# Optimization experiments

Hardware: AMD Instinct MI355X
Metric: run time of the kernel (lower is better)

Reference implementation:

```python
import jax, jax.numpy as jnp
import numpy as np

H = 16          # n_heads
DH = 128        # head_dim
DR = 64         # rope_dim
DC = DH - DR    # content_dim = 64
THETA = 10000.0
SCALE = 1.0 / np.sqrt(DH)


def _rope_tables(T, dtype):
    inv = 1.0 / (THETA ** (jnp.arange(0, DR, 2, dtype=jnp.float32) / DR))  # [DR/2]
    t = jnp.arange(T, dtype=jnp.float32)
    freqs = jnp.outer(t, inv)  # [T, DR/2]
    return jnp.cos(freqs).astype(dtype), jnp.sin(freqs).astype(dtype)


def _apply_rope(x, cos, sin):
    # x: [B,H,T,DR]; cos/sin: [T,DR/2] broadcast over B,H
    d = x.shape[-1] // 2
    x1, x2 = x[..., :d], x[..., d:]
    return jnp.concatenate([x1 * cos - x2 * sin, x1 * sin + x2 * cos], axis=-1)


def setup_inputs() -> dict:
    key = jax.random.key(0)
    ks = jax.random.split(key, 9)
    B, T, D = 1, 2048, 2048
    s = 0.02
    return {
        "x": jax.random.normal(ks[0], (B, T, D), jnp.float32),
        "Wq_down": jax.random.normal(ks[1], (D, 512), jnp.float32) * s,
        "Wq_up": jax.random.normal(ks[2], (512, H * DC), jnp.float32) * s,
        "Wq_rope": jax.random.normal(ks[3], (D, H * DR), jnp.float32) * s,
        "Wkv_down": jax.random.normal(ks[4], (D, 512), jnp.float32) * s,
        "Wk_up": jax.random.normal(ks[5], (512, H * DC), jnp.float32) * s,
        "Wv_up": jax.random.normal(ks[6], (512, H * DH), jnp.float32) * s,
        "Wk_rope": jax.random.normal(ks[7], (D, H * DR), jnp.float32) * s,
        "Wo": jax.random.normal(ks[8], (H * DH, D), jnp.float32) * s,
    }


def reference(x, Wq_down, Wq_up, Wq_rope, Wkv_down, Wk_up, Wv_up, Wk_rope, Wo):
    B, T, D = x.shape
    # low-rank query path: down then up, content part only
    q_content = ((x @ Wq_down) @ Wq_up).reshape(B, T, H, DC).transpose(0, 2, 1, 3)
    q_pos = (x @ Wq_rope).reshape(B, T, H, DR).transpose(0, 2, 1, 3)
    kv_latent = x @ Wkv_down                    # [B,T,d_latent]
    k_pos = (x @ Wk_rope).reshape(B, T, H, DR).transpose(0, 2, 1, 3)

    cos, sin = _rope_tables(T, x.dtype)
    q_pos = _apply_rope(q_pos, cos, sin)
    k_pos = _apply_rope(k_pos, cos, sin)

    k_content = (kv_latent @ Wk_up).reshape(B, T, H, DC).transpose(0, 2, 1, 3)
    v = (kv_latent @ Wv_up).reshape(B, T, H, DH).transpose(0, 2, 1, 3)

    q = jnp.concatenate([q_content, q_pos], axis=-1)  # [B,H,T,DH]
    k = jnp.concatenate([k_content, k_pos], axis=-1)  # [B,H,T,DH]

    scores = jnp.einsum("bhtd,bhsd->bhts", q, k) * SCALE
    causal = jnp.tril(jnp.ones((T, T), dtype=bool))
    scores = jnp.where(causal, scores, jnp.finfo(scores.dtype).min)
    attn = jax.nn.softmax(scores, axis=-1)
    out = jnp.einsum("bhts,bhsd->bhtd", attn, v)       # [B,H,T,DH]
    out = out.transpose(0, 2, 1, 3).reshape(B, T, H * DH)
    return out @ Wo
```

## Files before the change

kernel.cpp:

```cpp
#include <hip/hip_runtime.h>
#include <math.h>

#define T_SEQ 2048
#define D_MODEL 2048
#define H_HEADS 16
#define DH 128
#define DR 64
#define DC 64
#define D_LAT 512
#define NSPLIT 3
#define QSCALE (0.08838834764831845f * 1.4426950408889634f)

typedef __attribute__((ext_vector_type(8))) short short8;
typedef __attribute__((ext_vector_type(4))) short short4v;
typedef __attribute__((ext_vector_type(4))) float f32x4;

#if __has_builtin(__builtin_amdgcn_exp2f)
#define EXP2(x) __builtin_amdgcn_exp2f(x)
#else
#define EXP2(x) exp2f(x)
#endif

__device__ __forceinline__ float bf2f(short b) {
    unsigned u = ((unsigned)(unsigned short)b) << 16;
    return __builtin_bit_cast(float, u);
}
__device__ __forceinline__ short f2bf(float f) {
    unsigned u = __builtin_bit_cast(unsigned, f);
    unsigned r = u + 0x7fffu + ((u >> 16) & 1u);
    return (short)(r >> 16);
}
__device__ __forceinline__ short f2bf_trunc(float f) {
    return (short)(__builtin_bit_cast(unsigned, f) >> 16);
}

#define GLD_LDS(gp, lp) \
    __builtin_amdgcn_global_load_lds( \
        (const __attribute__((address_space(1))) void*)(gp), \
        (__attribute__((address_space(3))) void*)(lp), 16, 0, 0)

__device__ __forceinline__ void ct_tile(float (*tile)[33],
                                        const float* __restrict__ W,
                                        short* __restrict__ Wt,
                                        int R, int C, int ldo, int rel) {
    int bx = rel % (C / 32), by = rel / (C / 32);
    int c0 = bx * 32, r0 = by * 32;
    int tx = threadIdx.x & 31, ty = threadIdx.x >> 5;
    #pragma unroll
    for (int i = 0; i < 4; ++i)
        tile[ty + i * 8][tx] = W[(size_t)(r0 + ty + i * 8) * C + c0 + tx];
    __syncthreads();
    #pragma unroll
    for (int i = 0; i < 4; ++i)
        Wt[(size_t)(c0 + ty + i * 8) * ldo + r0 + tx] = f2bf(tile[tx][ty + i * 8]);
    __syncthreads();
}

__global__ __launch_bounds__(256) void prep(const float* __restrict__ x,
                                            short* __restrict__ xb,
                                            const float* __restrict__ Wqd,
                                            const float* __restrict__ Wkvd,
                                            const float* __restrict__ Wqr,
                                            const float* __restrict__ Wkr,
                                            const float* __restrict__ Wqu,
                                            const float* __restrict__ Wku,
                                            const float* __restrict__ Wvu,
                                            const float* __restrict__ Wo,
                                            short* __restrict__ WdT,
                                            short* __restrict__ WupT2,
                                            short* __restrict__ WoT) {
    __shared__ float tile[32][33];
    int bid = blockIdx.x;
    if (bid < 4096) {
        int i = bid * 1024 + threadIdx.x * 4;
        float4 f = *(const float4*)&x[i];
        short4v o;
        o.x = f2bf(f.x); o.y = f2bf(f.y); o.z = f2bf(f.z); o.w = f2bf(f.w);
        *(short4v*)&xb[i] = o;
    } else if (bid < 5120) {
        ct_tile(tile, Wqd,  WdT + (size_t)0 * 2048,    2048, 512,  2048, bid - 4096);
    } else if (bid < 6144) {
        ct_tile(tile, Wkvd, WdT + (size_t)512 * 2048,  2048, 512,  2048, bid - 5120);
    } else if (bid < 8192) {
        ct_tile(tile, Wqr,  WdT + (size_t)1024 * 2048, 2048, 1024, 2048, bid - 6144);
    } else if (bid < 10240) {
        ct_tile(tile, Wkr,  WdT + (size_t)2048 * 2048, 2048, 1024, 2048, bid - 8192);
    } else if (bid < 10752) {
        ct_tile(tile, Wqu,  WupT2 + (size_t)0 * 512,    512, 1024, 512, bid - 10240);
    } else if (bid < 11264) {
        ct_tile(tile, Wku,  WupT2 + (size_t)1024 * 512, 512, 1024, 512, bid - 10752);
    } else if (bid < 12288) {
        ct_tile(tile, Wvu,  WupT2 + (size_t)2048 * 512, 512, 2048, 512, bid - 11264);
    } else {
        ct_tile(tile, Wo,   WoT, 2048, 2048, 2048, bid - 12288);
    }
}

__global__ __launch_bounds__(256) void transpose_bf16(const short* __restrict__ in,
                                                      short* __restrict__ outb,
                                                      int ldi) {
    __shared__ short tile[64][65];
    int c0 = blockIdx.x * 64, t0 = blockIdx.y * 64;
    int tx = threadIdx.x & 31, ty = threadIdx.x >> 5;
    #pragma unroll
    for (int i = 0; i < 8; ++i) {
        int r = ty + i * 8;
        int vv = *(const int*)&in[(size_t)(t0 + r) * ldi + c0 + tx * 2];
        tile[r][tx * 2]     = (short)(vv & 0xffff);
        tile[r][tx * 2 + 1] = (short)(((unsigned)vv) >> 16);
    }
    __syncthreads();
    #pragma unroll
    for (int i = 0; i < 8; ++i) {
        int c = ty + i * 8;
        unsigned lo = (unsigned short)tile[tx * 2][c];
        unsigned hi = (unsigned short)tile[tx * 2 + 1][c];
        *(int*)&outb[(size_t)(c0 + c) * 2048 + t0 + tx * 2] = (int)(lo | (hi << 16));
    }
}

__global__ __launch_bounds__(256) void gemm_bt(const short* __restrict__ A,
                                               const short* __restrict__ A2,
                                               const short* __restrict__ Bt,
                                               short* __restrict__ C0,
                                               short* __restrict__ C1,
                                               short* __restrict__ C2,
                                               short* __restrict__ C3,
                                               int N, int Kblk,
                                               int lda, int ldb, int ldc,
                                               int ncut, int scut, float cscale) {
    __shared__ short As[128 * 32];
    __shared__ short Bs[128 * 32];
    const int tid = threadIdx.x;
    const int wave = tid >> 6, lane = tid & 63;
    const int lin = blockIdx.x;
    const int X = N >> 7, Xq = X >> 2;
    const int xcd = lin & 7;
    int r = lin >> 3;
    const int bx = (xcd & 3) * Xq + (r % Xq); r /= Xq;
    const int by = (xcd >> 2) * 8 + (r & 7);
    const int bz = r >> 3;
    const int row0 = by * 128, col0 = bx * 128;
    const int kbase = bz * Kblk;
    const short* Ause = (col0 < ncut) ? A : A2;
    short* Cuse = (bz == 0) ? C0 : (bz == 1) ? C1 : (bz == 2) ? C2 : C3;
    const int wr = (wave >> 1) * 64, wc = (wave & 1) * 64;
    const int lr = lane & 15, quad = lane >> 4;

    f32x4 acc[4][4];
    #pragma unroll
    for (int i = 0; i < 4; ++i)
        #pragma unroll
        for (int j = 0; j < 4; ++j) acc[i][j] = (f32x4){0.f, 0.f, 0.f, 0.f};

    for (int k0 = kbase; k0 < kbase + Kblk; k0 += 32) {
        __syncthreads();
        #pragma unroll
        for (int it = 0; it < 2; ++it) {
            int idx = wave * 64 + it * 256 + lane;
            const short* ga = Ause + (size_t)(row0 + (idx >> 2)) * lda + k0 + (idx & 3) * 8;
            const short* gb = Bt   + (size_t)(col0 + (idx >> 2)) * ldb + k0 + (idx & 3) * 8;
            int lds0 = (wave * 64 + it * 256) * 8;
            GLD_LDS(ga, &As[lds0]);
            GLD_LDS(gb, &Bs[lds0]);
        }
        __syncthreads();

        short8 af[4], bfr[4];
        #pragma unroll
        for (int i = 0; i < 4; ++i)
            af[i] = *(const short8*)&As[(wr + i * 16 + lr) * 32 + quad * 8];
        #pragma unroll
        for (int j = 0; j < 4; ++j)
            bfr[j] = *(const short8*)&Bs[(wc + j * 16 + lr) * 32 + quad * 8];
        #pragma unroll
        for (int i = 0; i < 4; ++i)
            #pragma unroll
            for (int j = 0; j < 4; ++j)
                acc[i][j] = __builtin_amdgcn_mfma_f32_16x16x32_bf16(af[i], bfr[j],
                                                                   acc[i][j], 0, 0, 0);
    }

    const float sc = (col0 < scut) ? cscale : 1.0f;
    #pragma unroll
    for (int i = 0; i < 4; ++i) {
        int rb = row0 + wr + i * 16 + quad * 4;
        #pragma unroll
        for (int j = 0; j < 4; ++j) {
            int c = col0 + wc + j * 16 + lr;
            #pragma unroll
            for (int rr = 0; rr < 4; ++rr)
                Cuse[(size_t)(rb + rr) * ldc + c] = f2bf(acc[i][j][rr] * sc);
        }
    }
}

__global__ __launch_bounds__(192) void finish_down(short* __restrict__ cat,
                                                   const short* __restrict__ pdown) {
    const int t = blockIdx.x;
    const int k8 = threadIdx.x * 8;
    const int c0 = ((k8 >> 5) << 6) + (k8 & 31);
    const size_t lo = (size_t)t * 3072 + c0;
    const size_t hi = lo + 32;
    short8 al = *(const short8*)&cat[lo];
    short8 ah = *(const short8*)&cat[hi];
    short8 bl = *(const short8*)&pdown[lo];
    short8 bh = *(const short8*)&pdown[hi];
    float xl[8], xh[8];
    #pragma unroll
    for (int j = 0; j < 8; ++j) {
        xl[j] = bf2f(al[j]) + bf2f(bl[j]);
        xh[j] = bf2f(ah[j]) + bf2f(bh[j]);
    }
    if (c0 >= 1024) {
        float sc = (c0 < 2048) ? QSCALE : 1.0f;
        #pragma unroll
        for (int j = 0; j < 8; ++j) {
            int i = (c0 & 31) + j;
            float freq = (float)t * __powf(10000.0f, -(float)i / 32.0f);
            float cs = cosf(freq), sn = sinf(freq);
            float r1 = (xl[j] * cs - xh[j] * sn) * sc;
            float r2 = (xl[j] * sn + xh[j] * cs) * sc;
            xl[j] = r1; xh[j] = r2;
        }
    }
    short8 ol, oh;
    #pragma unroll
    for (int j = 0; j < 8; ++j) { ol[j] = f2bf(xl[j]); oh[j] = f2bf(xh[j]); }
    *(short8*)&cat[lo] = ol;
    *(short8*)&cat[hi] = oh;
}

__global__ __launch_bounds__(256) void add_out_f32(const short* __restrict__ p0,
                                                   const short* __restrict__ p1,
                                                   const short* __restrict__ p2,
                                                   const short* __restrict__ p3,
                                                   float* __restrict__ out) {
    int i = (blockIdx.x * 256 + threadIdx.x) * 4;
    short4v a = *(const short4v*)&p0[i];
    short4v b = *(const short4v*)&p1[i];
    short4v c = *(const short4v*)&p2[i];
    short4v d = *(const short4v*)&p3[i];
    float4 o;
    o.x = (bf2f(a.x) + bf2f(b.x)) + (bf2f(c.x) + bf2f(d.x));
    o.y = (bf2f(a.y) + bf2f(b.y)) + (bf2f(c.y) + bf2f(d.y));
    o.z = (bf2f(a.z) + bf2f(b.z)) + (bf2f(c.z) + bf2f(d.z));
    o.w = (bf2f(a.w) + bf2f(b.w)) + (bf2f(c.w) + bf2f(d.w));
    *(float4*)&out[i] = o;
}

__global__ __launch_bounds__(256) void attn_mla_split(const short* __restrict__ qkup,
                                                      const short* __restrict__ cat,
                                                      const short* __restrict__ vT,
                                                      short* __restrict__ Opart01,
                                                      short* __restrict__ Opart2,
                                                      float* __restrict__ lpart) {
    const int lin = blockIdx.x;
    const int xcd = lin & 7;
    int r_ = lin >> 3;
    const int h = xcd + 8 * (r_ & 1);
    r_ >>= 1;
    const int qt = 31 - (r_ & 31);
    const int g = r_ >> 5;
    const int tid = threadIdx.x;
    const int wave = tid >> 6, lane = tid & 63;
    const int lr = lane & 15, quad = lane >> 4;

    __shared__ short Ks[32 * 128];
    __shared__ short Vst[128 * 32];
    __shared__ short Ps[4][16 * 40];

    short* Og = (g < 2) ? Opart01 + (size_t)g * (T_SEQ * 2048) : Opart2;
    const short8 ones = {0x3F80, 0x3F80, 0x3F80, 0x3F80,
                         0x3F80, 0x3F80, 0x3F80, 0x3F80};

    const int Q0 = qt * 64;
    const int qrow0 = Q0 + wave * 16;
    const int nchunk = 2 * qt + 2;
    const int qmax = qrow0 + 15;

    short8 qf[4];
    {
        int t = qrow0 + lr;
        #pragma unroll
        for (int kci = 0; kci < 4; ++kci) {
            const short* src = (kci < 2)
                ? qkup + (size_t)t * 4096 + h * 64
                : cat + (size_t)t * 3072 + 1024 + h * 64;
            qf[kci] = *(const short8*)&src[(kci & 1) * 32 + quad * 8];
        }
    }

    const int idx = wave * 64 + lane;
    const int key = idx >> 4;
    const int cg = (idx & 15) ^ (key & 15);
    const short* kp0 = (cg < 8)
        ? qkup + (size_t)key * 4096 + 1024 + h * 64 + cg * 8
        : cat + (size_t)key * 3072 + 2048 + h * 64 + (cg - 8) * 8;
    const int kst = (cg < 8) ? 4096 : 3072;
    const short* kp1 = kp0 + (size_t)16 * kst;
    const int dd = idx >> 2;
    const int scg = (idx & 3) ^ (dd & 3);
    const short* vp0 = vT + (size_t)(h * 128 + dd) * 2048 + scg * 8;
    const short* vp1 = vp0 + (size_t)64 * 2048;
    kp0 += (size_t)g * 32 * kst; kp1 += (size_t)g * 32 * kst;
    vp0 += g * 32;               vp1 += g * 32;
    const int kadv = NSPLIT * 32 * kst;
    const int vadv = NSPLIT * 32;
    const int ldsA = (wave * 64) * 8;
    const int ldsB = (wave * 64 + 256) * 8;

    f32x4 Oacc[8];
    #pragma unroll
    for (int d = 0; d < 8; ++d) Oacc[d] = (f32x4){0.f, 0.f, 0.f, 0.f};
    f32x4 Lacc = (f32x4){0.f, 0.f, 0.f, 0.f};

    for (int c = g; c < nchunk; c += NSPLIT) {
        const int s0 = c * 32;
        __syncthreads();
        GLD_LDS(kp0, &Ks[ldsA]);
        GLD_LDS(kp1, &Ks[ldsB]);
        GLD_LDS(vp0, &Vst[ldsA]);
        GLD_LDS(vp1, &Vst[ldsB]);
        kp0 += kadv; kp1 += kadv; vp0 += vadv; vp1 += vadv;
        __syncthreads();
        if (s0 > qmax) continue;

        f32x4 sacc[2];
        #pragma unroll
        for (int n = 0; n < 2; ++n) {
            sacc[n] = (f32x4){0.f, 0.f, 0.f, 0.f};
            #pragma unroll
            for (int kci = 0; kci < 4; ++kci) {
                short8 kf = *(const short8*)
                    &Ks[(n * 16 + lr) * 128 + ((kci * 4 + quad) ^ lr) * 8];
                sacc[n] = __builtin_amdgcn_mfma_f32_16x16x32_bf16(qf[kci], kf,
                                                                 sacc[n], 0, 0, 0);
            }
        }
        if (s0 + 31 > qrow0) {
            #pragma unroll
            for (int r = 0; r < 4; ++r) {
                int qg = qrow0 + quad * 4 + r;
                #pragma unroll
                for (int n = 0; n < 2; ++n) {
                    int s = s0 + n * 16 + lr;
                    sacc[n][r] = (s <= qg) ? sacc[n][r] : -1e30f;
                }
            }
        }
        #pragma unroll
        for (int r = 0; r < 4; ++r) {
            Ps[wave][(quad * 4 + r) * 40 + lr]      = f2bf_trunc(EXP2(sacc[0][r]));
            Ps[wave][(quad * 4 + r) * 40 + 16 + lr] = f2bf_trunc(EXP2(sacc[1][r]));
        }
        short8 pf = *(const short8*)&Ps[wave][lr * 40 + quad * 8];
        Lacc = __builtin_amdgcn_mfma_f32_16x16x32_bf16(pf, ones, Lacc, 0, 0, 0);
        #pragma unroll
        for (int dt = 0; dt < 8; ++dt) {
            short8 vf = *(const short8*)
                &Vst[(dt * 16 + lr) * 32 + (quad ^ (lr & 3)) * 8];
            Oacc[dt] = __builtin_amdgcn_mfma_f32_16x16x32_bf16(pf, vf,
                                                              Oacc[dt], 0, 0, 0);
        }
    }

    #pragma unroll
    for (int r = 0; r < 4; ++r) {
        int t = qrow0 + quad * 4 + r;
        #pragma unroll
        for (int dt = 0; dt < 8; ++dt)
            Og[(size_t)t * 2048 + h * 128 + dt * 16 + lr] = f2bf(Oacc[dt][r]);
    }
    if (lr == 0) {
        #pragma unroll
        for (int r = 0; r < 4; ++r) {
            int t = qrow0 + quad * 4 + r;
            lpart[(size_t)(g * T_SEQ + t) * H_HEADS + h] = Lacc[r];
        }
    }
}

__global__ __launch_bounds__(256) void attn_combine(const short* __restrict__ O01,
                                                    const short* __restrict__ O2,
                                                    const float* __restrict__ lpart,
                                                    short* __restrict__ ao) {
    const int t = blockIdx.x;
    const int h = threadIdx.x >> 4;
    const int di = (threadIdx.x & 15) * 8;
    size_t off = (size_t)t * 2048 + h * 128 + di;
    short8 a = *(const short8*)&O01[off];
    short8 b = *(const short8*)&O01[(size_t)T_SEQ * 2048 + off];
    short8 c = *(const short8*)&O2[off];
    float den = lpart[(size_t)(0 * T_SEQ + t) * H_HEADS + h] +
                lpart[(size_t)(1 * T_SEQ + t) * H_HEADS + h] +
                lpart[(size_t)(2 * T_SEQ + t) * H_HEADS + h];
    float inv = 1.0f / den;
    short8 o;
    #pragma unroll
    for (int j = 0; j < 8; ++j)
        o[j] = f2bf((bf2f(a[j]) + bf2f(b[j]) + bf2f(c[j])) * inv);
    *(short8*)&ao[off] = o;
}

extern "C" void kernel_launch(void* const* d_in, const int* in_sizes, int n_in,
                              void* d_out, int out_size, void* d_ws, size_t ws_size,
                              hipStream_t stream) {
    const float* x        = (const float*)d_in[0];
    const float* Wq_down  = (const float*)d_in[1];
    const float* Wq_up    = (const float*)d_in[2];
    const float* Wq_rope  = (const float*)d_in[3];
    const float* Wkv_down = (const float*)d_in[4];
    const float* Wk_up    = (const float*)d_in[5];
    const float* Wv_up    = (const float*)d_in[6];
    const float* Wk_rope  = (const float*)d_in[7];
    const float* Wo       = (const float*)d_in[8];
    float* out = (float*)d_out;

    short* p = (short*)d_ws;
    short* xb     = p; p += (size_t)2048 * 2048;
    short* WoT    = p; p += (size_t)2048 * 2048;
    short* cat    = p; p += (size_t)2048 * 3072;
    short* upcat2 = p; p += (size_t)2048 * 4096;
    short* WdT    = p; p += (size_t)3072 * 2048;
    short* WupT2  = p; p += (size_t)4096 * 512;
    short* vT     = p; p += (size_t)2048 * 2048;
    float* lpart  = (float*)p;
    short* pdown   = upcat2;
    short* aob     = cat;
    short* Opart01 = WdT;
    short* Opart2  = xb;
    short* pw0     = upcat2;
    short* pw1     = upcat2 + (size_t)2048 * 2048;
    short* pw2     = WdT;
    short* pw3     = WdT + (size_t)2048 * 2048;

    prep<<<dim3(16384), 256, 0, stream>>>(x, xb, Wq_down, Wkv_down, Wq_rope,
                                          Wk_rope, Wq_up, Wk_up, Wv_up, Wo,
                                          WdT, WupT2, WoT);

    gemm_bt<<<dim3(24 * 16 * 2), 256, 0, stream>>>(xb, xb, WdT, cat, pdown,
                                                   nullptr, nullptr,
                                                   3072, 1024,
                                                   2048, 2048, 3072, 1 << 30, 0, 1.f);

    finish_down<<<dim3(2048), 192, 0, stream>>>(cat, pdown);

    gemm_bt<<<dim3(32 * 16 * 1), 256, 0, stream>>>(cat, cat + 512, WupT2,
                                                   upcat2, nullptr, nullptr, nullptr,
                                                   4096, 512,
                                                   3072, 512, 4096, 1024, 1024, QSCALE);

    transpose_bf16<<<dim3(32, 32), 256, 0, stream>>>(upcat2 + 2048, vT, 4096);

    attn_mla_split<<<dim3(32 * 16 * NSPLIT), 256, 0, stream>>>(upcat2, cat, vT,
                                                               Opart01, Opart2, lpart);
    attn_combine<<<dim3(2048), 256, 0, stream>>>(Opart01, Opart2, lpart, aob);

    gemm_bt<<<dim3(16 * 16 * 4), 256, 0, stream>>>(aob, aob, WoT, pw0, pw1, pw2, pw3,
                                                   2048, 512,
                                                   2048, 2048, 2048, 1 << 30, 0, 1.f);
    add_out_f32<<<dim3(2048 * 2048 / 1024), 256, 0, stream>>>(pw0, pw1, pw2, pw3, out);
}
```

Measured before the change: 285.9 us.

## Process 128 query rows per attention block to reuse K/V tiles

The split attention kernel now gives each wave two 16-row query sub-blocks, so each block covers 128 query rows instead of 64 and the grid is halved. Every K/V chunk loaded into LDS then feeds twice the MFMA work, which cuts global and LDS traffic per unit of compute. In exchange it uses more registers for the doubled accumulators, launches fewer blocks, and idles the lower sub-block on diagonal chunks, which adds imbalance. The RoPE step also switches to fast intrinsic sin and cos, trading some accuracy for cheaper math.

```diff
diff --git a/kernel.cpp b/kernel.cpp
--- a/kernel.cpp
+++ b/kernel.cpp
@@ -218,7 +218,7 @@
         for (int j = 0; j < 8; ++j) {
             int i = (c0 & 31) + j;
             float freq = (float)t * __powf(10000.0f, -(float)i / 32.0f);
-            float cs = cosf(freq), sn = sinf(freq);
+            float cs = __cosf(freq), sn = __sinf(freq);
             float r1 = (xl[j] * cs - xh[j] * sn) * sc;
             float r2 = (xl[j] * sn + xh[j] * cs) * sc;
             xl[j] = r1; xh[j] = r2;
@@ -260,34 +260,35 @@
     int r_ = lin >> 3;
     const int h = xcd + 8 * (r_ & 1);
     r_ >>= 1;
-    const int qt = 31 - (r_ & 31);
-    const int g = r_ >> 5;
+    const int qt2 = 15 - (r_ & 15);
+    const int g = r_ >> 4;
     const int tid = threadIdx.x;
     const int wave = tid >> 6, lane = tid & 63;
     const int lr = lane & 15, quad = lane >> 4;
 
     __shared__ short Ks[32 * 128];
     __shared__ short Vst[128 * 32];
-    __shared__ short Ps[4][16 * 40];
+    __shared__ short Ps[4][2][16 * 40];
 
     short* Og = (g < 2) ? Opart01 + (size_t)g * (T_SEQ * 2048) : Opart2;
     const short8 ones = {0x3F80, 0x3F80, 0x3F80, 0x3F80,
                          0x3F80, 0x3F80, 0x3F80, 0x3F80};
 
-    const int Q0 = qt * 64;
-    const int qrow0 = Q0 + wave * 16;
-    const int nchunk = 2 * qt + 2;
-    const int qmax = qrow0 + 15;
-
-    short8 qf[4];
-    {
-        int t = qrow0 + lr;
+    const int Q0 = qt2 * 128;
+    const int qrowA = Q0 + wave * 16;
+    const int qrowB = qrowA + 64;
+    const int nchunk = 4 * qt2 + 4;
+
+    short8 qf[2][4];
+    #pragma unroll
+    for (int sb = 0; sb < 2; ++sb) {
+        int t = (sb ? qrowB : qrowA) + lr;
         #pragma unroll
         for (int kci = 0; kci < 4; ++kci) {
             const short* src = (kci < 2)
                 ? qkup + (size_t)t * 4096 + h * 64
                 : cat + (size_t)t * 3072 + 1024 + h * 64;
-            qf[kci] = *(const short8*)&src[(kci & 1) * 32 + quad * 8];
+            qf[sb][kci] = *(const short8*)&src[(kci & 1) * 32 + quad * 8];
         }
     }
 
@@ -310,10 +311,14 @@
     const int ldsA = (wave * 64) * 8;
     const int ldsB = (wave * 64 + 256) * 8;
 
-    f32x4 Oacc[8];
-    #pragma unroll
-    for (int d = 0; d < 8; ++d) Oacc[d] = (f32x4){0.f, 0.f, 0.f, 0.f};
-    f32x4 Lacc = (f32x4){0.f, 0.f, 0.f, 0.f};
+    f32x4 Oacc[2][8];
+    #pragma unroll
+    for (int sb = 0; sb < 2; ++sb)
+        #pragma unroll
+        for (int d = 0; d < 8; ++d) Oacc[sb][d] = (f32x4){0.f, 0.f, 0.f, 0.f};
+    f32x4 Lacc[2];
+    Lacc[0] = (f32x4){0.f, 0.f, 0.f, 0.f};
+    Lacc[1] = (f32x4){0.f, 0.f, 0.f, 0.f};
 
     for (int c = g; c < nchunk; c += NSPLIT) {
         const int s0 = c * 32;
@@ -324,59 +329,88 @@
         GLD_LDS(vp1, &Vst[ldsB]);
         kp0 += kadv; kp1 += kadv; vp0 += vadv; vp1 += vadv;
         __syncthreads();
-        if (s0 > qmax) continue;
-
-        f32x4 sacc[2];
+        if (s0 > qrowB + 15) continue;
+        const bool actA = (s0 <= qrowA + 15);
+
+        f32x4 sacc[2][2];
+        #pragma unroll
+        for (int sb = 0; sb < 2; ++sb)
+            #pragma unroll
+            for (int n = 0; n < 2; ++n) sacc[sb][n] = (f32x4){0.f, 0.f, 0.f, 0.f};
         #pragma unroll
         for (int n = 0; n < 2; ++n) {
-            sacc[n] = (f32x4){0.f, 0.f, 0.f, 0.f};
             #pragma unroll
             for (int kci = 0; kci < 4; ++kci) {
                 short8 kf = *(const short8*)
                     &Ks[(n * 16 + lr) * 128 + ((kci * 4 + quad) ^ lr) * 8];
-                sacc[n] = __builtin_amdgcn_mfma_f32_16x16x32_bf16(qf[kci], kf,
-                                                                 sacc[n], 0, 0, 0);
+                if (actA)
+                    sacc[0][n] = __builtin_amdgcn_mfma_f32_16x16x32_bf16(
+                        qf[0][kci], kf, sacc[0][n], 0, 0, 0);
+                sacc[1][n] = __builtin_amdgcn_mfma_f32_16x16x32_bf16(
+                    qf[1][kci], kf, sacc[1][n], 0, 0, 0);
             }
         }
-        if (s0 + 31 > qrow0) {
-            #pragma unroll
-            for (int r = 0; r < 4; ++r) {
-                int qg = qrow0 + quad * 4 + r;
+        #pragma unroll
+        for (int sb = 0; sb < 2; ++sb) {
+            if (sb == 0 && !actA) continue;
+            const int qrow0 = sb ? qrowB : qrowA;
+            if (s0 + 31 > qrow0) {
                 #pragma unroll
-                for (int n = 0; n < 2; ++n) {
-                    int s = s0 + n * 16 + lr;
-                    sacc[n][r] = (s <= qg) ? sacc[n][r] : -1e30f;
+                for (int r = 0; r < 4; ++r) {
+                    int qg = qrow0 + quad * 4 + r;
+                    #pragma unroll
+                    for (int n = 0; n < 2; ++n) {
+                        int s = s0 + n * 16 + lr;
+                        sacc[sb][n][r] = (s <= qg) ? sacc[sb][n][r] : -1e30f;
+                    }
                 }
             }
-        }
-        #pragma unroll
-        for (int r = 0; r < 4; ++r) {
-            Ps[wave][(quad * 4 + r) * 40 + lr]      = f2bf_trunc(EXP2(sacc[0][r]));
-            Ps[wave][(quad * 4 + r) * 40 + 16 + lr] = f2bf_trunc(EXP2(sacc[1][r]));
-        }
-        short8 pf = *(const short8*)&Ps[wave][lr * 40 + quad * 8];
-        Lacc = __builtin_amdgcn_mfma_f32_16x16x32_bf16(pf, ones, Lacc, 0, 0, 0);
+            #pragma unroll
+            for (int r = 0; r < 4; ++r) {
+                Ps[wave][sb][(quad * 4 + r) * 40 + lr] =
+                    f2bf_trunc(EXP2(sacc[sb][0][r]));
+                Ps[wave][sb][(quad * 4 + r) * 40 + 16 + lr] =
+                    f2bf_trunc(EXP2(sacc[sb][1][r]));
+            }
+        }
+        short8 pfA, pfB;
+        if (actA) {
+            pfA = *(const short8*)&Ps[wave][0][lr * 40 + quad * 8];
+            Lacc[0] = __builtin_amdgcn_mfma_f32_16x16x32_bf16(pfA, ones,
+                                                              Lacc[0], 0, 0, 0);
+        }
+        pfB = *(const short8*)&Ps[wave][1][lr * 40 + quad * 8];
+        Lacc[1] = __builtin_amdgcn_mfma_f32_16x16x32_bf16(pfB, ones,
+                                                          Lacc[1], 0, 0, 0);
         #pragma unroll
         for (int dt = 0; dt < 8; ++dt) {
             short8 vf = *(const short8*)
                 &Vst[(dt * 16 + lr) * 32 + (quad ^ (lr & 3)) * 8];
-            Oacc[dt] = __builtin_amdgcn_mfma_f32_16x16x32_bf16(pf, vf,
-                                                              Oacc[dt], 0, 0, 0);
-        }
-    }
-
-    #pragma unroll
-    for (int r = 0; r < 4; ++r) {
-        int t = qrow0 + quad * 4 + r;
-        #pragma unroll
-        for (int dt = 0; dt < 8; ++dt)
-            Og[(size_t)t * 2048 + h * 128 + dt * 16 + lr] = f2bf(Oacc[dt][r]);
-    }
-    if (lr == 0) {
+            if (actA)
+                Oacc[0][dt] = __builtin_amdgcn_mfma_f32_16x16x32_bf16(
+                    pfA, vf, Oacc[0][dt], 0, 0, 0);
+            Oacc[1][dt] = __builtin_amdgcn_mfma_f32_16x16x32_bf16(
+                pfB, vf, Oacc[1][dt], 0, 0, 0);
+        }
+    }
+
+    #pragma unroll
+    for (int sb = 0; sb < 2; ++sb) {
+        const int qrow0 = sb ? qrowB : qrowA;
         #pragma unroll
         for (int r = 0; r < 4; ++r) {
             int t = qrow0 + quad * 4 + r;
-            lpart[(size_t)(g * T_SEQ + t) * H_HEADS + h] = Lacc[r];
+            #pragma unroll
+            for (int dt = 0; dt < 8; ++dt)
+                Og[(size_t)t * 2048 + h * 128 + dt * 16 + lr] =
+                    f2bf(Oacc[sb][dt][r]);
+        }
+        if (lr == 0) {
+            #pragma unroll
+            for (int r = 0; r < 4; ++r) {
+                int t = qrow0 + quad * 4 + r;
+                lpart[(size_t)(g * T_SEQ + t) * H_HEADS + h] = Lacc[sb][r];
+            }
         }
     }
 }
@@ -453,7 +487,7 @@
 
     transpose_bf16<<<dim3(32, 32), 256, 0, stream>>>(upcat2 + 2048, vT, 4096);
 
-    attn_mla_split<<<dim3(32 * 16 * NSPLIT), 256, 0, stream>>>(upcat2, cat, vT,
+    attn_mla_split<<<dim3(16 * 16 * NSPLIT), 256, 0, stream>>>(upcat2, cat, vT,
                                                                Opart01, Opart2, lpart);
     attn_combine<<<dim3(2048), 256, 0, stream>>>(Opart01, Opart2, lpart, aob);
 
```

Result: no change. 282.9 us (-1.1%).
